# Kernel optimization log

Measured on AMD Instinct MI355X. Metric: run time of the kernel, lower is better.

The kernel has to match this reference:

```python
import jax, jax.numpy as jnp
import numpy as np

N, D, H, K = 131072, 512, 128, 3
NPOS, NNEG = 8192, 8192
KM_ITERS = 4
PROTO_SHIFT = 0.15
PROTO_LOGIT_SCALE = 0.2
TEMP = 2.5


def _sq_cdist(x, c):
    # squared euclidean distance, matches torch.cdist(...).pow(2)
    d = jnp.sum(x * x, -1, keepdims=True) + jnp.sum(c * c, -1)[None, :] - 2.0 * (x @ c.T)
    return jnp.maximum(d, 0.0)


def _kmeans(x, k, iters):
    # torch.linspace(0, n-1, steps=k).long() init, fixed iteration count
    n = x.shape[0]
    idx = jnp.linspace(0.0, n - 1, k).astype(jnp.int32)
    centers = x[idx]
    for _ in range(iters):
        assign = jnp.argmin(_sq_cdist(x, centers), axis=1)
        sums = jax.ops.segment_sum(x, assign, num_segments=k)
        counts = jax.ops.segment_sum(jnp.ones((n,), x.dtype), assign, num_segments=k)[:, None]
        # empty cluster keeps old center (mask.any() branch in torch)
        centers = jnp.where(counts > 0, sums / jnp.maximum(counts, 1.0), centers)
    return centers


def setup_inputs() -> dict:
    key = jax.random.key(0)
    ks = jax.random.split(key, 10)
    s = 1.0 / np.sqrt(D).astype(np.float32)
    return {
        "z_cls": jax.random.normal(ks[0], (N, D), jnp.float32),
        "z_proto": jax.random.normal(ks[1], (N, D), jnp.float32),
        "pos_ctx": jax.random.normal(ks[2], (D,), jnp.float32),
        "neg_ctx": jax.random.normal(ks[3], (D,), jnp.float32),
        "W1": jax.random.normal(ks[4], (H, D), jnp.float32) * s,
        "b1": jnp.zeros((H,), jnp.float32),
        "W2": jax.random.normal(ks[5], (1, H), jnp.float32) * (1.0 / np.sqrt(H).astype(np.float32)),
        "b2": jnp.zeros((1,), jnp.float32),
        "Wp": jax.random.normal(ks[6], (D, D), jnp.float32) * s,
        "bp": jnp.zeros((D,), jnp.float32),
        "Wn": jax.random.normal(ks[7], (D, D), jnp.float32) * s,
        "bn": jnp.zeros((D,), jnp.float32),
        "pos_idx": jax.random.randint(ks[8], (NPOS,), 0, N),
        "neg_idx": jax.random.randint(ks[9], (NNEG,), 0, N),
    }


def reference(z_cls, z_proto, pos_ctx, neg_ctx, W1, b1, W2, b2, Wp, bp, Wn, bn, pos_idx, neg_idx):
    # _build_prototypes (pos_idx/neg_idx nonempty path)
    pos_proto = _kmeans(z_proto[pos_idx], K, KM_ITERS)          # [K, D]
    neg_proto = jnp.mean(z_proto[neg_idx], axis=0)              # [D]
    # _calibrate (ema not initialized -> no EMA blend)
    pos_proto = pos_proto + PROTO_SHIFT * (pos_ctx @ Wp.T + bp)[None, :]
    neg_proto = neg_proto + PROTO_SHIFT * (neg_ctx @ Wn.T + bn)
    # distances
    d_pos_all = _sq_cdist(z_proto, pos_proto)                   # [N, K]
    d_pos = jnp.min(d_pos_all, axis=1)
    pos_assign = jnp.argmin(d_pos_all, axis=1)
    d_neg = jnp.mean((z_proto - neg_proto[None, :]) ** 2, axis=1)
    proto_logit = (d_neg - d_pos) / np.sqrt(D).astype(np.float32)
    # cls head (eval mode: dropout is identity)
    h = jax.nn.relu(z_cls @ W1.T + b1)
    cls_logit = (h @ W2.T + b2)[:, 0]
    logits = (cls_logit + PROTO_LOGIT_SCALE * proto_logit) / TEMP
    prob = jax.nn.sigmoid(logits)
    return (logits, prob, PROTO_LOGIT_SCALE * proto_logit, pos_assign, d_pos_all, pos_proto, neg_proto)
```

## Files before the change

### kernel.cpp

```cpp
#include <hip/hip_runtime.h>
#include <hip/hip_bf16.h>

#define NPTS 131072
#define DIM  512
#define HID  128
#define KCL  3
#define NPOSI 8192
#define NNEGI 8192

typedef __attribute__((ext_vector_type(8))) short bf16x8;
typedef __attribute__((ext_vector_type(4))) float f32x4;

enum {
  WS_SHIFT_POS = 0,
  WS_SHIFT_NEG = 512,
  WS_NEGSUM    = 1024,
  WS_NEGPART   = 1536,
  WS_SUMS      = 132608,
  WS_PPROTO    = 138764,
  WS_PN        = 140812,
  WS_W1FRAG    = 140816,
  WS_CLSL      = 173584,
};
#define SUMS_STRIDE 1539

__device__ __forceinline__ short f2bf(float x) {
  __hip_bfloat16 h = __float2bfloat16(x);
  return *reinterpret_cast<short*>(&h);
}

__global__ __launch_bounds__(256) void k_prep(const float* __restrict__ W1,
                                              const float* __restrict__ Wp, const float* __restrict__ bp,
                                              const float* __restrict__ Wn, const float* __restrict__ bn,
                                              const float* __restrict__ pos_ctx, const float* __restrict__ neg_ctx,
                                              const float* __restrict__ zp, const int* __restrict__ neg_idx,
                                              float* __restrict__ ws) {
  int bid = blockIdx.x, t = threadIdx.x;
  if (bid < 32) {
    int fid = bid * 256 + t;
    int kc = fid >> 9;
    int n  = (fid >> 6) & 7;
    int l  = fid & 63;
    int row = n * 16 + (l & 15);
    int col = kc * 32 + (l >> 4) * 8;
    const float* src = W1 + (size_t)row * DIM + col;
    float4 v0 = *(const float4*)(src);
    float4 v1 = *(const float4*)(src + 4);
    bf16x8 f;
    f[0] = f2bf(v0.x); f[1] = f2bf(v0.y); f[2] = f2bf(v0.z); f[3] = f2bf(v0.w);
    f[4] = f2bf(v1.x); f[5] = f2bf(v1.y); f[6] = f2bf(v1.z); f[7] = f2bf(v1.w);
    ((bf16x8*)(ws + WS_W1FRAG))[fid] = f;
  } else if (bid < 64) {
    int b = bid - 32;
    int mat = b >> 4;
    const float* W    = mat ? Wn : Wp;
    const float* bias = mat ? bn : bp;
    const float* ctx  = mat ? neg_ctx : pos_ctx;
    float* outp = ws + (mat ? WS_SHIFT_NEG : WS_SHIFT_POS);
    int row = (b & 15) * 32 + (t >> 3);
    int sub = t & 7;
    const float* wr = W + row * DIM + sub * 64;
    const float* cr = ctx + sub * 64;
    float s = 0.f;
#pragma unroll
    for (int j = 0; j < 64; j += 4) {
      float4 w4 = *(const float4*)(wr + j);
      float4 c4 = *(const float4*)(cr + j);
      s += w4.x * c4.x + w4.y * c4.y + w4.z * c4.z + w4.w * c4.w;
    }
    s += __shfl_xor(s, 1);
    s += __shfl_xor(s, 2);
    s += __shfl_xor(s, 4);
    if (sub == 0) outp[row] = 0.15f * (s + bias[row]);
  } else if (bid < 320) {
    int jb = bid - 64;
    int c0 = t * 2;
    float a0 = 0.f, a1 = 0.f;
    int base = jb * 32;
#pragma unroll 4
    for (int jj = 0; jj < 32; ++jj) {
      int row = neg_idx[base + jj];
      float2 v = *(const float2*)(zp + (size_t)row * DIM + c0);
      a0 += v.x; a1 += v.y;
    }
    ws[WS_NEGPART + jb * DIM + c0]     = a0;
    ws[WS_NEGPART + jb * DIM + c0 + 1] = a1;
  } else {
    for (int idx = t; idx < 4 * SUMS_STRIDE; idx += 256) ws[WS_SUMS + idx] = 0.f;
  }
}

template <int IT>
__global__ __launch_bounds__(256) void k_km(const float* __restrict__ zp,
                                            const int* __restrict__ pos_idx,
                                            float* __restrict__ ws) {
  int bid = blockIdx.x, t = threadIdx.x;
  if (IT == 0 && bid == 256) {
    int c0 = t * 2;
    float a0 = 0.f, a1 = 0.f;
#pragma unroll 8
    for (int j = 0; j < 256; ++j) {
      float2 v = *(const float2*)(ws + WS_NEGPART + j * DIM + c0);
      a0 += v.x; a1 += v.y;
    }
    ws[WS_NEGSUM + c0]     = a0;
    ws[WS_NEGSUM + c0 + 1] = a1;
    return;
  }
  __shared__ float cc[KCL * DIM];
  __shared__ float cn[KCL];
  __shared__ float lsum[KCL * DIM];
  __shared__ float lcnt[KCL];
  int w = t >> 6, l = t & 63;

  for (int idx = t; idx < KCL * DIM; idx += 256) lsum[idx] = 0.f;
  if (t < KCL) lcnt[t] = 0.f;

  for (int idx = t; idx < KCL * DIM; idx += 256) {
    int k = idx >> 9;
    int sel = (k == 0) ? 0 : ((k == 1) ? 4095 : 8191);
    float v = zp[(size_t)pos_idx[sel] * DIM + (idx & 511)];
#pragma unroll
    for (int j = 0; j < IT; ++j) {
      float cntv = ws[WS_SUMS + j * SUMS_STRIDE + 3 * DIM + k];
      float sv   = ws[WS_SUMS + j * SUMS_STRIDE + idx];
      v = (cntv > 0.f) ? sv / cntv : v;
    }
    cc[idx] = v;
  }
  __syncthreads();
  if (w < KCL) {
    float s = 0.f;
#pragma unroll
    for (int m = 0; m < 8; ++m) { float v = cc[w * DIM + l + m * 64]; s += v * v; }
#pragma unroll
    for (int m = 1; m < 64; m <<= 1) s += __shfl_xor(s, m);
    if (l == 0) cn[w] = s;
  }
  __syncthreads();

  float ck0[8], ck1[8], ck2[8];
#pragma unroll
  for (int j = 0; j < 8; ++j) {
    ck0[j] = cc[0 * DIM + l * 8 + j];
    ck1[j] = cc[1 * DIM + l * 8 + j];
    ck2[j] = cc[2 * DIM + l * 8 + j];
  }
  float cn0 = cn[0], cn1 = cn[1], cn2 = cn[2];
  float acc0[8] = {0,0,0,0,0,0,0,0}, acc1[8] = {0,0,0,0,0,0,0,0}, acc2[8] = {0,0,0,0,0,0,0,0};
  float cnt0 = 0.f, cnt1 = 0.f, cnt2 = 0.f;

  int wid = bid * 4 + w;
#pragma unroll 2
  for (int p = wid; p < NPOSI; p += 1024) {
    int row = pos_idx[p];
    const float* xr = zp + (size_t)row * DIM + l * 8;
    float4 x0 = *(const float4*)(xr);
    float4 x1 = *(const float4*)(xr + 4);
    float x[8] = {x0.x, x0.y, x0.z, x0.w, x1.x, x1.y, x1.z, x1.w};
    float d0 = 0.f, d1 = 0.f, d2 = 0.f;
#pragma unroll
    for (int j = 0; j < 8; ++j) { d0 += x[j] * ck0[j]; d1 += x[j] * ck1[j]; d2 += x[j] * ck2[j]; }
#pragma unroll
    for (int m = 1; m < 64; m <<= 1) {
      d0 += __shfl_xor(d0, m); d1 += __shfl_xor(d1, m); d2 += __shfl_xor(d2, m);
    }
    float t0 = cn0 - 2.f * d0, t1 = cn1 - 2.f * d1, t2 = cn2 - 2.f * d2;
    int a = 0; float best = t0;
    if (t1 < best) { best = t1; a = 1; }
    if (t2 < best) { best = t2; a = 2; }
    if (a == 0)      { cnt0 += 1.f;
#pragma unroll
      for (int j = 0; j < 8; ++j) acc0[j] += x[j]; }
    else if (a == 1) { cnt1 += 1.f;
#pragma unroll
      for (int j = 0; j < 8; ++j) acc1[j] += x[j]; }
    else             { cnt2 += 1.f;
#pragma unroll
      for (int j = 0; j < 8; ++j) acc2[j] += x[j]; }
  }
#pragma unroll
  for (int j = 0; j < 8; ++j) {
    atomicAdd(&lsum[0 * DIM + l * 8 + j], acc0[j]);
    atomicAdd(&lsum[1 * DIM + l * 8 + j], acc1[j]);
    atomicAdd(&lsum[2 * DIM + l * 8 + j], acc2[j]);
  }
  if (l == 0) {
    atomicAdd(&lcnt[0], cnt0); atomicAdd(&lcnt[1], cnt1); atomicAdd(&lcnt[2], cnt2);
  }
  __syncthreads();
  for (int idx = t; idx < KCL * DIM; idx += 256) atomicAdd(&ws[WS_SUMS + IT * SUMS_STRIDE + idx], lsum[idx]);
  if (t < KCL) atomicAdd(&ws[WS_SUMS + IT * SUMS_STRIDE + 3 * DIM + t], lcnt[t]);
}

__global__ __launch_bounds__(256) void k_fin(const float* __restrict__ zp,
                                             const int* __restrict__ pos_idx,
                                             float* __restrict__ ws,
                                             float* __restrict__ out) {
  __shared__ __align__(16) float pp[4 * DIM];
  int t = threadIdx.x, w = t >> 6, l = t & 63;
  for (int idx = t; idx < KCL * DIM; idx += 256) {
    int k = idx >> 9, d = idx & 511;
    int sel = (k == 0) ? 0 : ((k == 1) ? 4095 : 8191);
    float v = zp[(size_t)pos_idx[sel] * DIM + d];
#pragma unroll
    for (int j = 0; j < 4; ++j) {
      float cntv = ws[WS_SUMS + j * SUMS_STRIDE + 3 * DIM + k];
      float sv   = ws[WS_SUMS + j * SUMS_STRIDE + idx];
      v = (cntv > 0.f) ? sv / cntv : v;
    }
    pp[idx] = v + ws[WS_SHIFT_POS + d];
  }
  for (int d = t; d < DIM; d += 256)
    pp[3 * DIM + d] = ws[WS_NEGSUM + d] * (1.f / NNEGI) + ws[WS_SHIFT_NEG + d];
  __syncthreads();
  {
    float s = 0.f;
#pragma unroll
    for (int m = 0; m < 8; ++m) { float v = pp[w * DIM + l + m * 64]; s += v * v; }
#pragma unroll
    for (int m = 1; m < 64; m <<= 1) s += __shfl_xor(s, m);
    if (l == 0) ws[WS_PN + w] = s;
  }
  for (int idx = t; idx < 4 * DIM; idx += 256) {
    ws[WS_PPROTO + idx] = pp[idx];
    out[7 * NPTS + idx] = pp[idx];
  }
}

__global__ __launch_bounds__(256, 2) void k_cls(const float* __restrict__ zc,
                                                const float* __restrict__ b1,
                                                const float* __restrict__ W2,
                                                const float* __restrict__ b2,
                                                float* __restrict__ ws) {
  int t = threadIdx.x, w = t >> 6, l = t & 63;
  int i0 = blockIdx.x * 64;
  const bf16x8* w1f = (const bf16x8*)(ws + WS_W1FRAG);
  int arow = i0 + w * 16 + (l & 15);
  const float* aptr = zc + (size_t)arow * DIM + (l >> 4) * 8;

  f32x4 acc[8];
#pragma unroll
  for (int n = 0; n < 8; ++n) acc[n] = (f32x4){0.f, 0.f, 0.f, 0.f};

  float4 A[3][2];
  bf16x8 B[2][8];
#pragma unroll
  for (int s = 0; s < 3; ++s) {
    A[s][0] = *(const float4*)(aptr + s * 32);
    A[s][1] = *(const float4*)(aptr + s * 32 + 4);
  }
#pragma unroll
  for (int n = 0; n < 8; ++n) B[0][n] = w1f[n * 64 + l];

#pragma unroll
  for (int kc = 0; kc < 16; ++kc) {
    float4 a0 = A[kc % 3][0], a1 = A[kc % 3][1];
    bf16x8 af;
    af[0] = f2bf(a0.x); af[1] = f2bf(a0.y); af[2] = f2bf(a0.z); af[3] = f2bf(a0.w);
    af[4] = f2bf(a1.x); af[5] = f2bf(a1.y); af[6] = f2bf(a1.z); af[7] = f2bf(a1.w);
    if (kc + 3 < 16) {
      A[kc % 3][0] = *(const float4*)(aptr + (kc + 3) * 32);
      A[kc % 3][1] = *(const float4*)(aptr + (kc + 3) * 32 + 4);
    }
    if (kc + 1 < 16) {
#pragma unroll
      for (int n = 0; n < 8; ++n) B[(kc + 1) & 1][n] = w1f[(kc + 1) * 512 + n * 64 + l];
    }
#pragma unroll
    for (int n = 0; n < 8; ++n)
      acc[n] = __builtin_amdgcn_mfma_f32_16x16x32_bf16(af, B[kc & 1][n], acc[n], 0, 0, 0);
  }

  float p[4] = {0.f, 0.f, 0.f, 0.f};
  int col_l = l & 15;
#pragma unroll
  for (int n = 0; n < 8; ++n) {
    int col = n * 16 + col_l;
    float bb = b1[col], w2v = W2[col];
#pragma unroll
    for (int r = 0; r < 4; ++r) {
      float h = acc[n][r] + bb;
      h = h > 0.f ? h : 0.f;
      p[r] += h * w2v;
    }
  }
#pragma unroll
  for (int m = 1; m < 16; m <<= 1) {
#pragma unroll
    for (int r = 0; r < 4; ++r) p[r] += __shfl_xor(p[r], m);
  }
  if (col_l == 0) {
    float b2v = b2[0];
    int rbase = i0 + w * 16 + (l >> 4) * 4;
#pragma unroll
    for (int r = 0; r < 4; ++r) ws[WS_CLSL + rbase + r] = p[r] + b2v;
  }
}

__global__ __launch_bounds__(256, 4) void k_proto(const float* __restrict__ zp,
                                                  const float* __restrict__ ws,
                                                  float* __restrict__ out) {
  __shared__ __align__(16) float pp[4 * DIM];
  __shared__ float pns[4];
  int t = threadIdx.x;
  for (int idx = t; idx < 4 * DIM; idx += 256) pp[idx] = ws[WS_PPROTO + idx];
  if (t < 4) pns[t] = ws[WS_PN + t];
  __syncthreads();

  int w = t >> 6, l = t & 63, s = l & 7, r = l >> 3;
  int i = blockIdx.x * 32 + w * 8 + r;
  const float* xr = zp + (size_t)i * DIM;

  float d0 = 0.f, d1 = 0.f, d2 = 0.f, dn = 0.f, sx = 0.f;
#pragma unroll
  for (int j = 0; j < 16; ++j) {
    int col = j * 32 + s * 4;
    float4 x  = *(const float4*)(xr + col);
    float4 c0 = *(const float4*)(&pp[0 * DIM + col]);
    float4 c1 = *(const float4*)(&pp[1 * DIM + col]);
    float4 c2 = *(const float4*)(&pp[2 * DIM + col]);
    float4 c3 = *(const float4*)(&pp[3 * DIM + col]);
    d0 += x.x * c0.x + x.y * c0.y + x.z * c0.z + x.w * c0.w;
    d1 += x.x * c1.x + x.y * c1.y + x.z * c1.z + x.w * c1.w;
    d2 += x.x * c2.x + x.y * c2.y + x.z * c2.z + x.w * c2.w;
    dn += x.x * c3.x + x.y * c3.y + x.z * c3.z + x.w * c3.w;
    sx += x.x * x.x  + x.y * x.y  + x.z * x.z  + x.w * x.w;
  }
#pragma unroll
  for (int m = 1; m < 8; m <<= 1) {
    d0 += __shfl_xor(d0, m);
    d1 += __shfl_xor(d1, m);
    d2 += __shfl_xor(d2, m);
    dn += __shfl_xor(dn, m);
    sx += __shfl_xor(sx, m);
  }
  if (s == 0) {
    float e0 = sx + pns[0] - 2.f * d0; e0 = fmaxf(e0, 0.f);
    float e1 = sx + pns[1] - 2.f * d1; e1 = fmaxf(e1, 0.f);
    float e2 = sx + pns[2] - 2.f * d2; e2 = fmaxf(e2, 0.f);
    float dpos = e0; int a = 0;
    if (e1 < dpos) { dpos = e1; a = 1; }
    if (e2 < dpos) { dpos = e2; a = 2; }
    float dneg = (sx + pns[3] - 2.f * dn) * (1.f / DIM);
    float plog = (dneg - dpos) * 0.04419417382415922f;
    float o2 = 0.2f * plog;
    float lg = (ws[WS_CLSL + i] + o2) * 0.4f;
    float prob = 1.f / (1.f + expf(-lg));
    out[i]            = lg;
    out[NPTS + i]     = prob;
    out[2 * NPTS + i] = o2;
    out[3 * NPTS + i] = (float)a;
    out[4 * NPTS + 3 * i]     = e0;
    out[4 * NPTS + 3 * i + 1] = e1;
    out[4 * NPTS + 3 * i + 2] = e2;
  }
}

extern "C" void kernel_launch(void* const* d_in, const int* in_sizes, int n_in,
                              void* d_out, int out_size, void* d_ws, size_t ws_size,
                              hipStream_t stream) {
  const float* z_cls   = (const float*)d_in[0];
  const float* z_proto = (const float*)d_in[1];
  const float* pos_ctx = (const float*)d_in[2];
  const float* neg_ctx = (const float*)d_in[3];
  const float* W1      = (const float*)d_in[4];
  const float* b1      = (const float*)d_in[5];
  const float* W2      = (const float*)d_in[6];
  const float* b2      = (const float*)d_in[7];
  const float* Wp      = (const float*)d_in[8];
  const float* bp      = (const float*)d_in[9];
  const float* Wn      = (const float*)d_in[10];
  const float* bn      = (const float*)d_in[11];
  const int* pos_idx   = (const int*)d_in[12];
  const int* neg_idx   = (const int*)d_in[13];
  float* out           = (float*)d_out;
  float* ws            = (float*)d_ws;

  k_prep<<<321, 256, 0, stream>>>(W1, Wp, bp, Wn, bn, pos_ctx, neg_ctx, z_proto, neg_idx, ws);
  k_km<0><<<257, 256, 0, stream>>>(z_proto, pos_idx, ws);
  k_km<1><<<256, 256, 0, stream>>>(z_proto, pos_idx, ws);
  k_km<2><<<256, 256, 0, stream>>>(z_proto, pos_idx, ws);
  k_km<3><<<256, 256, 0, stream>>>(z_proto, pos_idx, ws);
  k_fin<<<1, 256, 0, stream>>>(z_proto, pos_idx, ws, out);
  k_cls<<<NPTS / 64, 256, 0, stream>>>(z_cls, b1, W2, b2, ws);
  k_proto<<<NPTS / 32, 256, 0, stream>>>(z_proto, ws, out);
}
```

Measured before the change: 276.1 us.

## Make k_cls persistent with LDS-staged W1, widen k-means grid, batch proto loads

k_cls now runs as 256 persistent blocks. Each block stages all W1 bf16 fragments in LDS once, loops over 8 row tiles, and keeps bias and W2 in registers. It is also launched right after prep instead of at the end. The k-means kernels double their grid to 512 blocks with deeper unrolling, and k_proto loads all 16 float4s of its row up front with lower launch-bound occupancy. The intent is to cut repeated global B-fragment loads and raise memory-level parallelism, at the cost of 128KB LDS per block and higher register pressure.

```diff
diff --git a/kernel.cpp b/kernel.cpp
--- a/kernel.cpp
+++ b/kernel.cpp
@@ -29,12 +29,12 @@
   return *reinterpret_cast<short*>(&h);
 }
 
-__global__ __launch_bounds__(256) void k_prep(const float* __restrict__ W1,
-                                              const float* __restrict__ Wp, const float* __restrict__ bp,
-                                              const float* __restrict__ Wn, const float* __restrict__ bn,
-                                              const float* __restrict__ pos_ctx, const float* __restrict__ neg_ctx,
-                                              const float* __restrict__ zp, const int* __restrict__ neg_idx,
-                                              float* __restrict__ ws) {
+__global__ __launch_bounds__(256, 1) void k_prep(const float* __restrict__ W1,
+                                                 const float* __restrict__ Wp, const float* __restrict__ bp,
+                                                 const float* __restrict__ Wn, const float* __restrict__ bn,
+                                                 const float* __restrict__ pos_ctx, const float* __restrict__ neg_ctx,
+                                                 const float* __restrict__ zp, const int* __restrict__ neg_idx,
+                                                 float* __restrict__ ws) {
   int bid = blockIdx.x, t = threadIdx.x;
   if (bid < 32) {
     int fid = bid * 256 + t;
@@ -77,7 +77,7 @@
     int c0 = t * 2;
     float a0 = 0.f, a1 = 0.f;
     int base = jb * 32;
-#pragma unroll 4
+#pragma unroll 8
     for (int jj = 0; jj < 32; ++jj) {
       int row = neg_idx[base + jj];
       float2 v = *(const float2*)(zp + (size_t)row * DIM + c0);
@@ -91,11 +91,11 @@
 }
 
 template <int IT>
-__global__ __launch_bounds__(256) void k_km(const float* __restrict__ zp,
-                                            const int* __restrict__ pos_idx,
-                                            float* __restrict__ ws) {
+__global__ __launch_bounds__(256, 1) void k_km(const float* __restrict__ zp,
+                                               const int* __restrict__ pos_idx,
+                                               float* __restrict__ ws) {
   int bid = blockIdx.x, t = threadIdx.x;
-  if (IT == 0 && bid == 256) {
+  if (IT == 0 && bid == 512) {
     int c0 = t * 2;
     float a0 = 0.f, a1 = 0.f;
 #pragma unroll 8
@@ -151,8 +151,8 @@
   float cnt0 = 0.f, cnt1 = 0.f, cnt2 = 0.f;
 
   int wid = bid * 4 + w;
-#pragma unroll 2
-  for (int p = wid; p < NPOSI; p += 1024) {
+#pragma unroll 4
+  for (int p = wid; p < NPOSI; p += 2048) {
     int row = pos_idx[p];
     const float* xr = zp + (size_t)row * DIM + l * 8;
     float4 x0 = *(const float4*)(xr);
@@ -228,77 +228,76 @@
   }
 }
 
-__global__ __launch_bounds__(256, 2) void k_cls(const float* __restrict__ zc,
+__global__ __launch_bounds__(256, 1) void k_cls(const float* __restrict__ zc,
                                                 const float* __restrict__ b1,
                                                 const float* __restrict__ W2,
                                                 const float* __restrict__ b2,
                                                 float* __restrict__ ws) {
+  __shared__ bf16x8 Bs[8192];
   int t = threadIdx.x, w = t >> 6, l = t & 63;
-  int i0 = blockIdx.x * 64;
   const bf16x8* w1f = (const bf16x8*)(ws + WS_W1FRAG);
-  int arow = i0 + w * 16 + (l & 15);
-  const float* aptr = zc + (size_t)arow * DIM + (l >> 4) * 8;
-
-  f32x4 acc[8];
-#pragma unroll
-  for (int n = 0; n < 8; ++n) acc[n] = (f32x4){0.f, 0.f, 0.f, 0.f};
-
-  float4 A[3][2];
-  bf16x8 B[2][8];
-#pragma unroll
-  for (int s = 0; s < 3; ++s) {
-    A[s][0] = *(const float4*)(aptr + s * 32);
-    A[s][1] = *(const float4*)(aptr + s * 32 + 4);
-  }
-#pragma unroll
-  for (int n = 0; n < 8; ++n) B[0][n] = w1f[n * 64 + l];
-
-#pragma unroll
-  for (int kc = 0; kc < 16; ++kc) {
-    float4 a0 = A[kc % 3][0], a1 = A[kc % 3][1];
-    bf16x8 af;
-    af[0] = f2bf(a0.x); af[1] = f2bf(a0.y); af[2] = f2bf(a0.z); af[3] = f2bf(a0.w);
-    af[4] = f2bf(a1.x); af[5] = f2bf(a1.y); af[6] = f2bf(a1.z); af[7] = f2bf(a1.w);
-    if (kc + 3 < 16) {
-      A[kc % 3][0] = *(const float4*)(aptr + (kc + 3) * 32);
-      A[kc % 3][1] = *(const float4*)(aptr + (kc + 3) * 32 + 4);
-    }
-    if (kc + 1 < 16) {
-#pragma unroll
-      for (int n = 0; n < 8; ++n) B[(kc + 1) & 1][n] = w1f[(kc + 1) * 512 + n * 64 + l];
-    }
-#pragma unroll
-    for (int n = 0; n < 8; ++n)
-      acc[n] = __builtin_amdgcn_mfma_f32_16x16x32_bf16(af, B[kc & 1][n], acc[n], 0, 0, 0);
-  }
-
-  float p[4] = {0.f, 0.f, 0.f, 0.f};
+#pragma unroll 4
+  for (int idx = t; idx < 8192; idx += 256) Bs[idx] = w1f[idx];
+
   int col_l = l & 15;
-#pragma unroll
-  for (int n = 0; n < 8; ++n) {
-    int col = n * 16 + col_l;
-    float bb = b1[col], w2v = W2[col];
-#pragma unroll
-    for (int r = 0; r < 4; ++r) {
-      float h = acc[n][r] + bb;
-      h = h > 0.f ? h : 0.f;
-      p[r] += h * w2v;
-    }
-  }
-#pragma unroll
-  for (int m = 1; m < 16; m <<= 1) {
-#pragma unroll
-    for (int r = 0; r < 4; ++r) p[r] += __shfl_xor(p[r], m);
-  }
-  if (col_l == 0) {
-    float b2v = b2[0];
-    int rbase = i0 + w * 16 + (l >> 4) * 4;
-#pragma unroll
-    for (int r = 0; r < 4; ++r) ws[WS_CLSL + rbase + r] = p[r] + b2v;
-  }
-}
-
-__global__ __launch_bounds__(256, 4) void k_proto(const float* __restrict__ zp,
+  float b1c[8], w2c[8];
+#pragma unroll
+  for (int n = 0; n < 8; ++n) { b1c[n] = b1[n * 16 + col_l]; w2c[n] = W2[n * 16 + col_l]; }
+  float b2v = b2[0];
+  __syncthreads();
+
+  for (int tile = 0; tile < 8; ++tile) {
+    int i0 = (blockIdx.x * 8 + tile) * 64;
+    const float* aptr = zc + (size_t)(i0 + w * 16 + (l & 15)) * DIM + (l >> 4) * 8;
+
+    f32x4 acc[8];
+#pragma unroll
+    for (int n = 0; n < 8; ++n) acc[n] = (f32x4){0.f, 0.f, 0.f, 0.f};
+
+    float4 A[8][2];
+#pragma unroll
+    for (int s = 0; s < 8; ++s) {
+      A[s][0] = *(const float4*)(aptr + s * 32);
+      A[s][1] = *(const float4*)(aptr + s * 32 + 4);
+    }
+#pragma unroll
+    for (int kc = 0; kc < 16; ++kc) {
+      float4 a0 = A[kc & 7][0], a1 = A[kc & 7][1];
+      if (kc < 8) {
+        A[kc][0] = *(const float4*)(aptr + (kc + 8) * 32);
+        A[kc][1] = *(const float4*)(aptr + (kc + 8) * 32 + 4);
+      }
+      bf16x8 af;
+      af[0] = f2bf(a0.x); af[1] = f2bf(a0.y); af[2] = f2bf(a0.z); af[3] = f2bf(a0.w);
+      af[4] = f2bf(a1.x); af[5] = f2bf(a1.y); af[6] = f2bf(a1.z); af[7] = f2bf(a1.w);
+#pragma unroll
+      for (int n = 0; n < 8; ++n)
+        acc[n] = __builtin_amdgcn_mfma_f32_16x16x32_bf16(af, Bs[kc * 512 + n * 64 + l], acc[n], 0, 0, 0);
+    }
+    float p[4] = {0.f, 0.f, 0.f, 0.f};
+#pragma unroll
+    for (int n = 0; n < 8; ++n) {
+#pragma unroll
+      for (int r = 0; r < 4; ++r) {
+        float h = acc[n][r] + b1c[n];
+        h = h > 0.f ? h : 0.f;
+        p[r] += h * w2c[n];
+      }
+    }
+#pragma unroll
+    for (int m = 1; m < 16; m <<= 1) {
+#pragma unroll
+      for (int r = 0; r < 4; ++r) p[r] += __shfl_xor(p[r], m);
+    }
+    if (col_l == 0) {
+      int rbase = i0 + w * 16 + (l >> 4) * 4;
+#pragma unroll
+      for (int r = 0; r < 4; ++r) ws[WS_CLSL + rbase + r] = p[r] + b2v;
+    }
+  }
+}
+
+__global__ __launch_bounds__(256, 2) void k_proto(const float* __restrict__ zp,
                                                   const float* __restrict__ ws,
                                                   float* __restrict__ out) {
   __shared__ __align__(16) float pp[4 * DIM];
@@ -312,20 +311,23 @@
   int i = blockIdx.x * 32 + w * 8 + r;
   const float* xr = zp + (size_t)i * DIM;
 
+  float4 x[16];
+#pragma unroll
+  for (int j = 0; j < 16; ++j) x[j] = *(const float4*)(xr + j * 32 + s * 4);
+
   float d0 = 0.f, d1 = 0.f, d2 = 0.f, dn = 0.f, sx = 0.f;
 #pragma unroll
   for (int j = 0; j < 16; ++j) {
     int col = j * 32 + s * 4;
-    float4 x  = *(const float4*)(xr + col);
     float4 c0 = *(const float4*)(&pp[0 * DIM + col]);
     float4 c1 = *(const float4*)(&pp[1 * DIM + col]);
     float4 c2 = *(const float4*)(&pp[2 * DIM + col]);
     float4 c3 = *(const float4*)(&pp[3 * DIM + col]);
-    d0 += x.x * c0.x + x.y * c0.y + x.z * c0.z + x.w * c0.w;
-    d1 += x.x * c1.x + x.y * c1.y + x.z * c1.z + x.w * c1.w;
-    d2 += x.x * c2.x + x.y * c2.y + x.z * c2.z + x.w * c2.w;
-    dn += x.x * c3.x + x.y * c3.y + x.z * c3.z + x.w * c3.w;
-    sx += x.x * x.x  + x.y * x.y  + x.z * x.z  + x.w * x.w;
+    d0 += x[j].x * c0.x + x[j].y * c0.y + x[j].z * c0.z + x[j].w * c0.w;
+    d1 += x[j].x * c1.x + x[j].y * c1.y + x[j].z * c1.z + x[j].w * c1.w;
+    d2 += x[j].x * c2.x + x[j].y * c2.y + x[j].z * c2.z + x[j].w * c2.w;
+    dn += x[j].x * c3.x + x[j].y * c3.y + x[j].z * c3.z + x[j].w * c3.w;
+    sx += x[j].x * x[j].x + x[j].y * x[j].y + x[j].z * x[j].z + x[j].w * x[j].w;
   }
 #pragma unroll
   for (int m = 1; m < 8; m <<= 1) {
@@ -378,11 +380,11 @@
   float* ws            = (float*)d_ws;
 
   k_prep<<<321, 256, 0, stream>>>(W1, Wp, bp, Wn, bn, pos_ctx, neg_ctx, z_proto, neg_idx, ws);
-  k_km<0><<<257, 256, 0, stream>>>(z_proto, pos_idx, ws);
-  k_km<1><<<256, 256, 0, stream>>>(z_proto, pos_idx, ws);
-  k_km<2><<<256, 256, 0, stream>>>(z_proto, pos_idx, ws);
-  k_km<3><<<256, 256, 0, stream>>>(z_proto, pos_idx, ws);
+  k_cls<<<256, 256, 0, stream>>>(z_cls, b1, W2, b2, ws);
+  k_km<0><<<513, 256, 0, stream>>>(z_proto, pos_idx, ws);
+  k_km<1><<<512, 256, 0, stream>>>(z_proto, pos_idx, ws);
+  k_km<2><<<512, 256, 0, stream>>>(z_proto, pos_idx, ws);
+  k_km<3><<<512, 256, 0, stream>>>(z_proto, pos_idx, ws);
   k_fin<<<1, 256, 0, stream>>>(z_proto, pos_idx, ws, out);
-  k_cls<<<NPTS / 64, 256, 0, stream>>>(z_cls, b1, W2, b2, ws);
   k_proto<<<NPTS / 32, 256, 0, stream>>>(z_proto, ws, out);
 }
```

New measurement: 370.2 us. 1.34x slower.

## Pre-gather positive rows, stage cls A-tiles in LDS, restructure proto kernel

Applied to the files above, without the earlier changes.

Positive-sample rows are gathered once in the prep kernel into a contiguous workspace buffer, so the four k-means passes read contiguous memory instead of doing indexed gathers. K-means now uses 512 blocks, each warp handling four rows loaded up front. The cls kernel converts its z_cls tile to bf16 in LDS with coalesced row loads before the MFMA loop, and uses a swizzled block order. The proto kernel gives each warp 8 full rows with per-lane centroid registers and full-wave reductions, and the launch order moves k_cls ahead of k-means. The cost is an extra 16 MB workspace copy plus heavier shuffle and register use.

```diff
diff --git a/kernel.cpp b/kernel.cpp
--- a/kernel.cpp
+++ b/kernel.cpp
@@ -21,6 +21,7 @@
   WS_PN        = 140812,
   WS_W1FRAG    = 140816,
   WS_CLSL      = 173584,
+  WS_POSG      = 304656,
 };
 #define SUMS_STRIDE 1539
 
@@ -33,7 +34,8 @@
                                               const float* __restrict__ Wp, const float* __restrict__ bp,
                                               const float* __restrict__ Wn, const float* __restrict__ bn,
                                               const float* __restrict__ pos_ctx, const float* __restrict__ neg_ctx,
-                                              const float* __restrict__ zp, const int* __restrict__ neg_idx,
+                                              const float* __restrict__ zp,
+                                              const int* __restrict__ neg_idx, const int* __restrict__ pos_idx,
                                               float* __restrict__ ws) {
   int bid = blockIdx.x, t = threadIdx.x;
   if (bid < 32) {
@@ -77,7 +79,7 @@
     int c0 = t * 2;
     float a0 = 0.f, a1 = 0.f;
     int base = jb * 32;
-#pragma unroll 4
+#pragma unroll 8
     for (int jj = 0; jj < 32; ++jj) {
       int row = neg_idx[base + jj];
       float2 v = *(const float2*)(zp + (size_t)row * DIM + c0);
@@ -85,17 +87,35 @@
     }
     ws[WS_NEGPART + jb * DIM + c0]     = a0;
     ws[WS_NEGPART + jb * DIM + c0 + 1] = a1;
+  } else if (bid < 448) {
+    int j = bid - 320;
+    int w = t >> 6, l = t & 63;
+    int row0 = j * 64 + w * 16;
+#pragma unroll
+    for (int rb = 0; rb < 16; rb += 4) {
+      float4 a[4], b[4];
+#pragma unroll
+      for (int r = 0; r < 4; ++r) {
+        const float* src = zp + (size_t)pos_idx[row0 + rb + r] * DIM + l * 8;
+        a[r] = *(const float4*)(src);
+        b[r] = *(const float4*)(src + 4);
+      }
+#pragma unroll
+      for (int r = 0; r < 4; ++r) {
+        float* dst = ws + WS_POSG + (size_t)(row0 + rb + r) * DIM + l * 8;
+        *(float4*)(dst)     = a[r];
+        *(float4*)(dst + 4) = b[r];
+      }
+    }
   } else {
     for (int idx = t; idx < 4 * SUMS_STRIDE; idx += 256) ws[WS_SUMS + idx] = 0.f;
   }
 }
 
 template <int IT>
-__global__ __launch_bounds__(256) void k_km(const float* __restrict__ zp,
-                                            const int* __restrict__ pos_idx,
-                                            float* __restrict__ ws) {
+__global__ __launch_bounds__(256, 1) void k_km(float* __restrict__ ws) {
   int bid = blockIdx.x, t = threadIdx.x;
-  if (IT == 0 && bid == 256) {
+  if (IT == 0 && bid == 512) {
     int c0 = t * 2;
     float a0 = 0.f, a1 = 0.f;
 #pragma unroll 8
@@ -119,7 +139,7 @@
   for (int idx = t; idx < KCL * DIM; idx += 256) {
     int k = idx >> 9;
     int sel = (k == 0) ? 0 : ((k == 1) ? 4095 : 8191);
-    float v = zp[(size_t)pos_idx[sel] * DIM + (idx & 511)];
+    float v = ws[WS_POSG + (size_t)sel * DIM + (idx & 511)];
 #pragma unroll
     for (int j = 0; j < IT; ++j) {
       float cntv = ws[WS_SUMS + j * SUMS_STRIDE + 3 * DIM + k];
@@ -150,14 +170,17 @@
   float acc0[8] = {0,0,0,0,0,0,0,0}, acc1[8] = {0,0,0,0,0,0,0,0}, acc2[8] = {0,0,0,0,0,0,0,0};
   float cnt0 = 0.f, cnt1 = 0.f, cnt2 = 0.f;
 
-  int wid = bid * 4 + w;
-#pragma unroll 2
-  for (int p = wid; p < NPOSI; p += 1024) {
-    int row = pos_idx[p];
-    const float* xr = zp + (size_t)row * DIM + l * 8;
-    float4 x0 = *(const float4*)(xr);
-    float4 x1 = *(const float4*)(xr + 4);
-    float x[8] = {x0.x, x0.y, x0.z, x0.w, x1.x, x1.y, x1.z, x1.w};
+  int p0 = (bid * 4 + w) * 4;
+  const float* xbase = ws + WS_POSG + (size_t)p0 * DIM + l * 8;
+  float4 xa[4], xb[4];
+#pragma unroll
+  for (int r = 0; r < 4; ++r) {
+    xa[r] = *(const float4*)(xbase + r * DIM);
+    xb[r] = *(const float4*)(xbase + r * DIM + 4);
+  }
+#pragma unroll
+  for (int r = 0; r < 4; ++r) {
+    float x[8] = {xa[r].x, xa[r].y, xa[r].z, xa[r].w, xb[r].x, xb[r].y, xb[r].z, xb[r].w};
     float d0 = 0.f, d1 = 0.f, d2 = 0.f;
 #pragma unroll
     for (int j = 0; j < 8; ++j) { d0 += x[j] * ck0[j]; d1 += x[j] * ck1[j]; d2 += x[j] * ck2[j]; }
@@ -193,16 +216,13 @@
   if (t < KCL) atomicAdd(&ws[WS_SUMS + IT * SUMS_STRIDE + 3 * DIM + t], lcnt[t]);
 }
 
-__global__ __launch_bounds__(256) void k_fin(const float* __restrict__ zp,
-                                             const int* __restrict__ pos_idx,
-                                             float* __restrict__ ws,
-                                             float* __restrict__ out) {
+__global__ __launch_bounds__(256) void k_fin(float* __restrict__ ws, float* __restrict__ out) {
   __shared__ __align__(16) float pp[4 * DIM];
   int t = threadIdx.x, w = t >> 6, l = t & 63;
   for (int idx = t; idx < KCL * DIM; idx += 256) {
     int k = idx >> 9, d = idx & 511;
     int sel = (k == 0) ? 0 : ((k == 1) ? 4095 : 8191);
-    float v = zp[(size_t)pos_idx[sel] * DIM + d];
+    float v = ws[WS_POSG + (size_t)sel * DIM + d];
 #pragma unroll
     for (int j = 0; j < 4; ++j) {
       float cntv = ws[WS_SUMS + j * SUMS_STRIDE + 3 * DIM + k];
@@ -228,41 +248,47 @@
   }
 }
 
-__global__ __launch_bounds__(256, 2) void k_cls(const float* __restrict__ zc,
-                                                const float* __restrict__ b1,
-                                                const float* __restrict__ W2,
-                                                const float* __restrict__ b2,
-                                                float* __restrict__ ws) {
+__global__ __launch_bounds__(256) void k_cls(const float* __restrict__ zc,
+                                             const float* __restrict__ b1,
+                                             const float* __restrict__ W2,
+                                             const float* __restrict__ b2,
+                                             float* __restrict__ ws) {
+  __shared__ bf16x8 Abuf[4096];
   int t = threadIdx.x, w = t >> 6, l = t & 63;
-  int i0 = blockIdx.x * 64;
+  int bid = (blockIdx.x & 7) * 256 + (blockIdx.x >> 3);
+  int i0 = bid * 64;
   const bf16x8* w1f = (const bf16x8*)(ws + WS_W1FRAG);
-  int arow = i0 + w * 16 + (l & 15);
-  const float* aptr = zc + (size_t)arow * DIM + (l >> 4) * 8;
+  bf16x8* ab = Abuf + w * 1024;
+  const float* arow = zc + (size_t)(i0 + w * 16) * DIM + l * 8;
+
+#pragma unroll
+  for (int Rb = 0; Rb < 16; Rb += 8) {
+    float4 La[8], Lb[8];
+#pragma unroll
+    for (int r = 0; r < 8; ++r) {
+      La[r] = *(const float4*)(arow + (size_t)(Rb + r) * DIM);
+      Lb[r] = *(const float4*)(arow + (size_t)(Rb + r) * DIM + 4);
+    }
+#pragma unroll
+    for (int r = 0; r < 8; ++r) {
+      int R = Rb + r;
+      bf16x8 ch;
+      ch[0] = f2bf(La[r].x); ch[1] = f2bf(La[r].y); ch[2] = f2bf(La[r].z); ch[3] = f2bf(La[r].w);
+      ch[4] = f2bf(Lb[r].x); ch[5] = f2bf(Lb[r].y); ch[6] = f2bf(Lb[r].z); ch[7] = f2bf(Lb[r].w);
+      ab[(l >> 2) * 64 + R + ((l & 3) << 4)] = ch;
+    }
+  }
 
   f32x4 acc[8];
 #pragma unroll
   for (int n = 0; n < 8; ++n) acc[n] = (f32x4){0.f, 0.f, 0.f, 0.f};
-
-  float4 A[3][2];
   bf16x8 B[2][8];
 #pragma unroll
-  for (int s = 0; s < 3; ++s) {
-    A[s][0] = *(const float4*)(aptr + s * 32);
-    A[s][1] = *(const float4*)(aptr + s * 32 + 4);
-  }
-#pragma unroll
   for (int n = 0; n < 8; ++n) B[0][n] = w1f[n * 64 + l];
 
 #pragma unroll
   for (int kc = 0; kc < 16; ++kc) {
-    float4 a0 = A[kc % 3][0], a1 = A[kc % 3][1];
-    bf16x8 af;
-    af[0] = f2bf(a0.x); af[1] = f2bf(a0.y); af[2] = f2bf(a0.z); af[3] = f2bf(a0.w);
-    af[4] = f2bf(a1.x); af[5] = f2bf(a1.y); af[6] = f2bf(a1.z); af[7] = f2bf(a1.w);
-    if (kc + 3 < 16) {
-      A[kc % 3][0] = *(const float4*)(aptr + (kc + 3) * 32);
-      A[kc % 3][1] = *(const float4*)(aptr + (kc + 3) * 32 + 4);
-    }
+    bf16x8 af = ab[kc * 64 + l];
     if (kc + 1 < 16) {
 #pragma unroll
       for (int n = 0; n < 8; ++n) B[(kc + 1) & 1][n] = w1f[(kc + 1) * 512 + n * 64 + l];
@@ -298,9 +324,9 @@
   }
 }
 
-__global__ __launch_bounds__(256, 4) void k_proto(const float* __restrict__ zp,
-                                                  const float* __restrict__ ws,
-                                                  float* __restrict__ out) {
+__global__ __launch_bounds__(256) void k_proto(const float* __restrict__ zp,
+                                               const float* __restrict__ ws,
+                                               float* __restrict__ out) {
   __shared__ __align__(16) float pp[4 * DIM];
   __shared__ float pns[4];
   int t = threadIdx.x;
@@ -308,52 +334,78 @@
   if (t < 4) pns[t] = ws[WS_PN + t];
   __syncthreads();
 
-  int w = t >> 6, l = t & 63, s = l & 7, r = l >> 3;
-  int i = blockIdx.x * 32 + w * 8 + r;
-  const float* xr = zp + (size_t)i * DIM;
-
-  float d0 = 0.f, d1 = 0.f, d2 = 0.f, dn = 0.f, sx = 0.f;
-#pragma unroll
-  for (int j = 0; j < 16; ++j) {
-    int col = j * 32 + s * 4;
-    float4 x  = *(const float4*)(xr + col);
-    float4 c0 = *(const float4*)(&pp[0 * DIM + col]);
-    float4 c1 = *(const float4*)(&pp[1 * DIM + col]);
-    float4 c2 = *(const float4*)(&pp[2 * DIM + col]);
-    float4 c3 = *(const float4*)(&pp[3 * DIM + col]);
-    d0 += x.x * c0.x + x.y * c0.y + x.z * c0.z + x.w * c0.w;
-    d1 += x.x * c1.x + x.y * c1.y + x.z * c1.z + x.w * c1.w;
-    d2 += x.x * c2.x + x.y * c2.y + x.z * c2.z + x.w * c2.w;
-    dn += x.x * c3.x + x.y * c3.y + x.z * c3.z + x.w * c3.w;
-    sx += x.x * x.x  + x.y * x.y  + x.z * x.z  + x.w * x.w;
-  }
-#pragma unroll
-  for (int m = 1; m < 8; m <<= 1) {
-    d0 += __shfl_xor(d0, m);
-    d1 += __shfl_xor(d1, m);
-    d2 += __shfl_xor(d2, m);
-    dn += __shfl_xor(dn, m);
-    sx += __shfl_xor(sx, m);
-  }
-  if (s == 0) {
-    float e0 = sx + pns[0] - 2.f * d0; e0 = fmaxf(e0, 0.f);
-    float e1 = sx + pns[1] - 2.f * d1; e1 = fmaxf(e1, 0.f);
-    float e2 = sx + pns[2] - 2.f * d2; e2 = fmaxf(e2, 0.f);
+  int w = t >> 6, l = t & 63;
+  int bid = (blockIdx.x & 7) * 512 + (blockIdx.x >> 3);
+  int r0 = (bid * 4 + w) * 8;
+  const float* base = zp + (size_t)r0 * DIM + l * 8;
+
+  float c0v[8], c1v[8], c2v[8], c3v[8];
+#pragma unroll
+  for (int j = 0; j < 8; ++j) {
+    c0v[j] = pp[0 * DIM + l * 8 + j];
+    c1v[j] = pp[1 * DIM + l * 8 + j];
+    c2v[j] = pp[2 * DIM + l * 8 + j];
+    c3v[j] = pp[3 * DIM + l * 8 + j];
+  }
+  float pn0 = pns[0], pn1 = pns[1], pn2 = pns[2], nn = pns[3];
+
+  float4 xa[8], xb[8];
+#pragma unroll
+  for (int rr = 0; rr < 8; ++rr) {
+    xa[rr] = *(const float4*)(base + rr * DIM);
+    xb[rr] = *(const float4*)(base + rr * DIM + 4);
+  }
+
+  float r_lg = 0.f, r_pr = 0.f, r_o2 = 0.f, r_as = 0.f, r_e0 = 0.f, r_e1 = 0.f, r_e2 = 0.f;
+#pragma unroll
+  for (int rr = 0; rr < 8; ++rr) {
+    float x[8] = {xa[rr].x, xa[rr].y, xa[rr].z, xa[rr].w, xb[rr].x, xb[rr].y, xb[rr].z, xb[rr].w};
+    float d0 = 0.f, d1 = 0.f, d2 = 0.f, dn = 0.f, sx = 0.f;
+#pragma unroll
+    for (int j = 0; j < 8; ++j) {
+      d0 += x[j] * c0v[j];
+      d1 += x[j] * c1v[j];
+      d2 += x[j] * c2v[j];
+      dn += x[j] * c3v[j];
+      sx += x[j] * x[j];
+    }
+#pragma unroll
+    for (int m = 1; m < 64; m <<= 1) {
+      d0 += __shfl_xor(d0, m);
+      d1 += __shfl_xor(d1, m);
+      d2 += __shfl_xor(d2, m);
+      dn += __shfl_xor(dn, m);
+      sx += __shfl_xor(sx, m);
+    }
+    float e0 = sx + pn0 - 2.f * d0; e0 = fmaxf(e0, 0.f);
+    float e1 = sx + pn1 - 2.f * d1; e1 = fmaxf(e1, 0.f);
+    float e2 = sx + pn2 - 2.f * d2; e2 = fmaxf(e2, 0.f);
     float dpos = e0; int a = 0;
     if (e1 < dpos) { dpos = e1; a = 1; }
     if (e2 < dpos) { dpos = e2; a = 2; }
-    float dneg = (sx + pns[3] - 2.f * dn) * (1.f / DIM);
+    float dneg = (sx + nn - 2.f * dn) * (1.f / DIM);
     float plog = (dneg - dpos) * 0.04419417382415922f;
     float o2 = 0.2f * plog;
-    float lg = (ws[WS_CLSL + i] + o2) * 0.4f;
+    float lg = (ws[WS_CLSL + r0 + rr] + o2) * 0.4f;
     float prob = 1.f / (1.f + expf(-lg));
-    out[i]            = lg;
-    out[NPTS + i]     = prob;
-    out[2 * NPTS + i] = o2;
-    out[3 * NPTS + i] = (float)a;
-    out[4 * NPTS + 3 * i]     = e0;
-    out[4 * NPTS + 3 * i + 1] = e1;
-    out[4 * NPTS + 3 * i + 2] = e2;
+    bool sel = (l == rr);
+    r_lg = sel ? lg : r_lg;
+    r_pr = sel ? prob : r_pr;
+    r_o2 = sel ? o2 : r_o2;
+    r_as = sel ? (float)a : r_as;
+    r_e0 = sel ? e0 : r_e0;
+    r_e1 = sel ? e1 : r_e1;
+    r_e2 = sel ? e2 : r_e2;
+  }
+  if (l < 8) {
+    int i = r0 + l;
+    out[i]            = r_lg;
+    out[NPTS + i]     = r_pr;
+    out[2 * NPTS + i] = r_o2;
+    out[3 * NPTS + i] = r_as;
+    out[4 * NPTS + 3 * i]     = r_e0;
+    out[4 * NPTS + 3 * i + 1] = r_e1;
+    out[4 * NPTS + 3 * i + 2] = r_e2;
   }
 }
 
@@ -377,12 +429,12 @@
   float* out           = (float*)d_out;
   float* ws            = (float*)d_ws;
 
-  k_prep<<<321, 256, 0, stream>>>(W1, Wp, bp, Wn, bn, pos_ctx, neg_ctx, z_proto, neg_idx, ws);
-  k_km<0><<<257, 256, 0, stream>>>(z_proto, pos_idx, ws);
-  k_km<1><<<256, 256, 0, stream>>>(z_proto, pos_idx, ws);
-  k_km<2><<<256, 256, 0, stream>>>(z_proto, pos_idx, ws);
-  k_km<3><<<256, 256, 0, stream>>>(z_proto, pos_idx, ws);
-  k_fin<<<1, 256, 0, stream>>>(z_proto, pos_idx, ws, out);
+  k_prep<<<449, 256, 0, stream>>>(W1, Wp, bp, Wn, bn, pos_ctx, neg_ctx, z_proto, neg_idx, pos_idx, ws);
   k_cls<<<NPTS / 64, 256, 0, stream>>>(z_cls, b1, W2, b2, ws);
+  k_km<0><<<513, 256, 0, stream>>>(ws);
+  k_km<1><<<512, 256, 0, stream>>>(ws);
+  k_km<2><<<512, 256, 0, stream>>>(ws);
+  k_km<3><<<512, 256, 0, stream>>>(ws);
+  k_fin<<<1, 256, 0, stream>>>(ws, out);
   k_proto<<<NPTS / 32, 256, 0, stream>>>(z_proto, ws, out);
 }
```

Measured after the change: 293.7 us. 1.06x slower.
